# Optimization experiments

Hardware: AMD Instinct MI355X
Metric: run time of the kernel (lower is better)

## Reference

```python
import jax, jax.numpy as jnp
import numpy as np

H = 16  # num_heads
LN_EPS = 1e-5


def setup_inputs() -> dict:
    key = jax.random.key(0)
    ks = jax.random.split(key, 9)
    B, T, D = 2, 2048, 1024
    s = D ** -0.5
    return {
        "q": jax.random.normal(ks[0], (B, T, D), jnp.float32),
        "k": jax.random.normal(ks[1], (B, T, D), jnp.float32),
        "v": jax.random.normal(ks[2], (B, T, D), jnp.float32),
        "wq": jax.random.normal(ks[3], (D, D), jnp.float32) * s,
        "bq": jnp.zeros((D,), jnp.float32),
        "wk": jax.random.normal(ks[4], (D, D), jnp.float32) * s,
        "bk": jnp.zeros((D,), jnp.float32),
        "wv": jax.random.normal(ks[5], (D, D), jnp.float32) * s,
        "bv": jnp.zeros((D,), jnp.float32),
        "ln_g": jnp.ones((D,), jnp.float32),
        "ln_b": jnp.zeros((D,), jnp.float32),
    }


def _layernorm(x, g, b):
    mu = jnp.mean(x, axis=-1, keepdims=True)
    var = jnp.mean(jnp.square(x - mu), axis=-1, keepdims=True)
    return (x - mu) * jax.lax.rsqrt(var + LN_EPS) * g + b


def reference(q, k, v, wq, bq, wk, bk, wv, bv, ln_g, ln_b):
    B, T, D = q.shape
    dh = D // H
    residual = q
    qp = q @ wq.T + bq
    kp = k @ wk.T + bk
    vp = v @ wv.T + bv
    # faithful to torch: flat row-major view (B,T,D) -> (H*B, T, dh)
    qh = qp.reshape(H * B, T, dh)
    kh = kp.reshape(H * B, T, dh)
    vh = vp.reshape(H * B, T, dh)
    scores = jnp.einsum('btd,bsd->bts', qh, kh) * (dh ** -0.5)  # (H*B, T, T)
    attn = jax.nn.softmax(scores, axis=-1)
    ctx = jnp.einsum('bts,bsd->btd', attn, vh)  # (H*B, T, dh)
    ctx = ctx.reshape(B, T, D)
    out = _layernorm(residual + ctx, ln_g, ln_b)
    return (out, attn)
```

## Files before the change

### kernel.cpp

```cpp
#include <hip/hip_runtime.h>

typedef unsigned short u16;
typedef __attribute__((ext_vector_type(8))) short s8v;
typedef __attribute__((ext_vector_type(4))) float f4v;

#define MFMA16(a, b, c) __builtin_amdgcn_mfma_f32_16x16x32_bf16(a, b, c, 0, 0, 0)

#define TSEQ 2048
#define NTOK 4096
#define HEADS 32
#define HB_ELEMS 131072

__device__ __forceinline__ unsigned cvt_pk(float lo, float hi) {
  unsigned r;
  asm("v_cvt_pk_bf16_f32 %0, %1, %2" : "=v"(r) : "v"(lo), "v"(hi));
  return r;
}

__device__ __forceinline__ void gl_lds16(const u16* g, u16* l) {
  __builtin_amdgcn_global_load_lds(
      (const __attribute__((address_space(1))) void*)g,
      (__attribute__((address_space(3))) void*)l, 16, 0, 0);
}

__global__ void cvt_all(const float* __restrict__ q, const float* __restrict__ k,
                        const float* __restrict__ v, const float* __restrict__ wq,
                        const float* __restrict__ wk, const float* __restrict__ wv,
                        u16* __restrict__ dst) {
  int i = (blockIdx.x * blockDim.x + threadIdx.x) * 4;
  const float* src; int off;
  if (i < 12582912) {
    int s = i >> 22; src = (s == 0) ? q : ((s == 1) ? k : v); off = i & 4194303;
  } else {
    int j = i - 12582912;
    int s = j >> 20; src = (s == 0) ? wq : ((s == 1) ? wk : wv); off = j & 1048575;
  }
  float4 val = *(const float4*)(src + off);
  uint2 o;
  o.x = cvt_pk(val.x, val.y);
  o.y = cvt_pk(val.z, val.w);
  *(uint2*)(dst + i) = o;
}

__launch_bounds__(256, 3)
__global__ void proj_gemm(const u16* __restrict__ Aall, const u16* __restrict__ Wall,
                          const float* __restrict__ bqp, const float* __restrict__ bkp,
                          const float* __restrict__ bvp, u16* __restrict__ Call) {
  const int z = blockIdx.z;
  const u16* A = Aall + (size_t)z * 4194304;
  const u16* W = Wall + (size_t)z * 1048576;
  u16* C = Call + (size_t)z * 4194304;
  const float* bias = (z == 0) ? bqp : ((z == 1) ? bkp : bvp);

  __shared__ __align__(16) u16 SH[17408];
  u16* As = SH;
  u16* Bs = SH + 8192;

  const int tid = threadIdx.x;
  const int w = tid >> 6, lane = tid & 63, g = lane >> 4, l = lane & 15;
  const int wr = w >> 1, wc = w & 1;
  const int tr = blockIdx.y * 128, tc = blockIdx.x * 128;

  const int srow = tid >> 3;
  const int scol = (tid & 7) * 8;

  f4v acc[4][4] = {};

  for (int kt = 0; kt < 1024; kt += 64) {
#pragma unroll
    for (int c4 = 0; c4 < 4; ++c4) {
      gl_lds16(A + (size_t)(tr + c4 * 32 + srow) * 1024 + kt + scol,
               As + c4 * 2048 + tid * 8);
      gl_lds16(W + (size_t)(tc + c4 * 32 + srow) * 1024 + kt + scol,
               Bs + c4 * 2048 + tid * 8);
    }
    __syncthreads();
#pragma unroll
    for (int ks = 0; ks < 2; ++ks) {
      s8v a[4], bb[4];
#pragma unroll
      for (int m = 0; m < 4; ++m)
        a[m] = *(const s8v*)(As + (wr * 64 + m * 16 + l) * 64 + ks * 32 + g * 8);
#pragma unroll
      for (int n = 0; n < 4; ++n)
        bb[n] = *(const s8v*)(Bs + (wc * 64 + n * 16 + l) * 64 + ks * 32 + g * 8);
#pragma unroll
      for (int m = 0; m < 4; ++m)
#pragma unroll
        for (int n = 0; n < 4; ++n)
          acc[m][n] = MFMA16(a[m], bb[n], acc[m][n]);
    }
    __syncthreads();
  }
  u16* T = SH;
#pragma unroll
  for (int m = 0; m < 4; ++m)
#pragma unroll
    for (int n = 0; n < 4; ++n) {
      int d = wc * 64 + n * 16 + l;
      float bv = bias[tc + d];
      unsigned c01 = cvt_pk(acc[m][n][0] + bv, acc[m][n][1] + bv);
      unsigned c23 = cvt_pk(acc[m][n][2] + bv, acc[m][n][3] + bv);
      int t0 = wr * 64 + m * 16 + g * 4;
      T[(t0 + 0) * 136 + d] = (u16)c01;
      T[(t0 + 1) * 136 + d] = (u16)(c01 >> 16);
      T[(t0 + 2) * 136 + d] = (u16)c23;
      T[(t0 + 3) * 136 + d] = (u16)(c23 >> 16);
    }
  __syncthreads();
#pragma unroll
  for (int it = 0; it < 8; ++it) {
    int t = it * 16 + (tid >> 4);
    int c8 = (tid & 15) * 8;
    *(s8v*)(C + (size_t)(tr + t) * 1024 + tc + c8) = *(const s8v*)&T[t * 136 + c8];
  }
}

__global__ void vtrans(const u16* __restrict__ vp, u16* __restrict__ vT) {
  const int hb = blockIdx.y;
  const int t0 = blockIdx.x * 64;
  const int tid = threadIdx.x;
  __shared__ u16 tl[64][65];
  const u16* vph = vp + (size_t)hb * HB_ELEMS;
  u16* vth = vT + (size_t)hb * HB_ELEMS;
#pragma unroll
  for (int it = 0; it < 4; ++it) {
    int i = (tid + it * 256) * 4;
    int r = i >> 6, c = i & 63;
    *(ushort4*)&tl[r][c] = *(const ushort4*)(vph + (size_t)(t0 + r) * 64 + c);
  }
  __syncthreads();
#pragma unroll
  for (int it = 0; it < 4; ++it) {
    int i = (tid + it * 256) * 4;
    int d = i >> 6, j = i & 63;
    ushort4 o;
    o.x = tl[j + 0][d]; o.y = tl[j + 1][d]; o.z = tl[j + 2][d]; o.w = tl[j + 3][d];
    *(ushort4*)(vth + (size_t)d * TSEQ + t0 + j) = o;
  }
}

__launch_bounds__(512, 2)
__global__ void attn_fused(const u16* __restrict__ qp, const u16* __restrict__ kp,
                           const u16* __restrict__ vT, float* __restrict__ attn,
                           float* __restrict__ ctx) {
  const int hw = blockIdx.x + (blockIdx.y << 4);
  const int hb = (hw & 7) + ((hw >> 7) << 3);
  const int qt = (hw >> 3) & 15;

  const int tid = threadIdx.x;
  const int w = tid >> 6, lane = tid & 63, g = lane >> 4, l = lane & 15;
  const int lx = l & 7;

  const u16* qh = qp + (size_t)hb * HB_ELEMS;
  const u16* kh = kp + (size_t)hb * HB_ELEMS;
  const u16* vh = vT + (size_t)hb * HB_ELEMS;

  __shared__ __align__(16) u16 SH[27648];

  const int row0 = qt * 128 + w * 16;
  const float scale = 0.125f;

  const int srow = tid >> 3;
  const int swc = ((tid & 7) ^ (srow & 7)) * 8;

  s8v qf0 = *(const s8v*)(qh + (size_t)(row0 + l) * 64 + g * 8);
  s8v qf1 = *(const s8v*)(qh + (size_t)(row0 + l) * 64 + 32 + g * 8);

  float sum = 0.0f;
  for (int kt4 = 0; kt4 < 8; ++kt4) {
    const int c0 = kt4 * 256;
#pragma unroll
    for (int c4 = 0; c4 < 4; ++c4)
      gl_lds16(kh + (size_t)(c0 + c4 * 64 + srow) * 64 + swc,
               SH + c4 * 4096 + tid * 8);
    __syncthreads();
#pragma unroll
    for (int q4 = 0; q4 < 4; ++q4) {
#pragma unroll
      for (int n = 0; n < 4; ++n) {
        const u16* kr = SH + q4 * 4096 + (n * 16 + l) * 64;
        s8v b0 = *(const s8v*)(kr + (g ^ lx) * 8);
        s8v b1 = *(const s8v*)(kr + ((4 + g) ^ lx) * 8);
        f4v s = {};
        s = MFMA16(b0, qf0, s);
        s = MFMA16(b1, qf1, s);
        sum += __expf(s[0] * scale) + __expf(s[1] * scale)
             + __expf(s[2] * scale) + __expf(s[3] * scale);
      }
    }
    __syncthreads();
  }
  sum += __shfl_xor(sum, 16);
  sum += __shfl_xor(sum, 32);
  const float inv = 1.0f / sum;

  u16* Kl = SH;
  u16* Vl = SH + 4096;
  float* Pf = (float*)(SH + 8192);

  f4v cacc[4] = {};
  float* attn_h = attn + (size_t)hb * TSEQ * TSEQ;
  const int kt0 = (qt * 2 + ((hw >> 7) << 3)) & 31;
  const int prow = w * 16 + l;
  const int st_r = tid >> 4;
  const int st_c = (tid & 15) * 4;
  for (int i = 0; i < 32; ++i) {
    const int kt = (i + kt0) & 31;
    const int col0 = kt * 64;
    gl_lds16(kh + (size_t)(col0 + srow) * 64 + swc, Kl + tid * 8);
    gl_lds16(vh + (size_t)srow * TSEQ + col0 + swc, Vl + tid * 8);
    __syncthreads();
#pragma unroll
    for (int n = 0; n < 4; ++n) {
      const u16* kr = Kl + (n * 16 + l) * 64;
      s8v b0 = *(const s8v*)(kr + (g ^ lx) * 8);
      s8v b1 = *(const s8v*)(kr + ((4 + g) ^ lx) * 8);
      f4v s = {};
      s = MFMA16(b0, qf0, s);
      s = MFMA16(b1, qf1, s);
      f4v p;
#pragma unroll
      for (int r = 0; r < 4; ++r) p[r] = __expf(s[r] * scale) * inv;
      *(f4v*)&Pf[prow * 76 + n * 16 + g * 4] = p;
    }
    asm volatile("s_waitcnt lgkmcnt(0)" ::: "memory");
    __builtin_amdgcn_sched_barrier(0);
#pragma unroll
    for (int ks = 0; ks < 2; ++ks) {
      const float* pr = &Pf[prow * 76 + ks * 32 + g * 8];
      f4v r0 = *(const f4v*)pr;
      f4v r1 = *(const f4v*)(pr + 4);
      union { unsigned u[4]; s8v s; } pc;
      pc.u[0] = cvt_pk(r0[0], r0[1]);
      pc.u[1] = cvt_pk(r0[2], r0[3]);
      pc.u[2] = cvt_pk(r1[0], r1[1]);
      pc.u[3] = cvt_pk(r1[2], r1[3]);
      s8v pa = pc.s;
#pragma unroll
      for (int n4 = 0; n4 < 4; ++n4) {
        const u16* vr = Vl + (n4 * 16 + l) * 64;
        s8v bvv = *(const s8v*)(vr + ((ks * 4 + g) ^ lx) * 8);
        cacc[n4] = MFMA16(pa, bvv, cacc[n4]);
      }
    }
    __syncthreads();
#pragma unroll
    for (int r4 = 0; r4 < 4; ++r4) {
      const int rho = r4 * 32 + st_r;
      f4v pv_ = *(const f4v*)&Pf[rho * 76 + st_c];
      *(f4v*)(attn_h + (size_t)(qt * 128 + rho) * TSEQ + col0 + st_c) = pv_;
    }
  }
#pragma unroll
  for (int n4 = 0; n4 < 4; ++n4)
#pragma unroll
    for (int r = 0; r < 4; ++r)
      ctx[(size_t)hb * HB_ELEMS + (size_t)(row0 + g * 4 + r) * 64 + n4 * 16 + l] =
          cacc[n4][r];
}

__global__ void ln_kernel(const float* __restrict__ q, const float* __restrict__ ctx,
                          const float* __restrict__ gam, const float* __restrict__ bet,
                          float* __restrict__ out) {
  const int row = blockIdx.x;
  const int tid = threadIdx.x;
  const float* qr = q + (size_t)row * 1024;
  const float* cr = ctx + (size_t)row * 1024;
  float4 xq = *(const float4*)(qr + tid * 4);
  float4 xc = *(const float4*)(cr + tid * 4);
  float x0 = xq.x + xc.x, x1 = xq.y + xc.y, x2 = xq.z + xc.z, x3 = xq.w + xc.w;
  float s1 = x0 + x1 + x2 + x3;
  float s2 = x0 * x0 + x1 * x1 + x2 * x2 + x3 * x3;
#pragma unroll
  for (int off = 1; off < 64; off <<= 1) {
    s1 += __shfl_xor(s1, off);
    s2 += __shfl_xor(s2, off);
  }
  __shared__ float ra[4], rb[4];
  int w = tid >> 6, lane = tid & 63;
  if (lane == 0) { ra[w] = s1; rb[w] = s2; }
  __syncthreads();
  s1 = ra[0] + ra[1] + ra[2] + ra[3];
  s2 = rb[0] + rb[1] + rb[2] + rb[3];
  float mu = s1 * (1.0f / 1024.0f);
  float var = s2 * (1.0f / 1024.0f) - mu * mu;
  float rstd = rsqrtf(var + 1e-5f);
  float4 gv = *(const float4*)(gam + tid * 4);
  float4 bv = *(const float4*)(bet + tid * 4);
  float4 o;
  o.x = (x0 - mu) * rstd * gv.x + bv.x;
  o.y = (x1 - mu) * rstd * gv.y + bv.y;
  o.z = (x2 - mu) * rstd * gv.z + bv.z;
  o.w = (x3 - mu) * rstd * gv.w + bv.w;
  *(float4*)(out + (size_t)row * 1024 + tid * 4) = o;
}

extern "C" void kernel_launch(void* const* d_in, const int* in_sizes, int n_in,
                              void* d_out, int out_size, void* d_ws, size_t ws_size,
                              hipStream_t stream) {
  const float* q    = (const float*)d_in[0];
  const float* k    = (const float*)d_in[1];
  const float* v    = (const float*)d_in[2];
  const float* wq   = (const float*)d_in[3];
  const float* bq   = (const float*)d_in[4];
  const float* wk   = (const float*)d_in[5];
  const float* bk   = (const float*)d_in[6];
  const float* wv   = (const float*)d_in[7];
  const float* bv   = (const float*)d_in[8];
  const float* ln_g = (const float*)d_in[9];
  const float* ln_b = (const float*)d_in[10];

  char* ws = (char*)d_ws;
  u16* qbf  = (u16*)(ws);
  u16* wbf  = (u16*)(ws + 25165824);
  u16* qp   = (u16*)(ws + 31457280);
  u16* vT   = (u16*)(ws + 56623104);
  float* ctx = (float*)(ws + 65011712);

  float* out  = (float*)d_out;
  float* attn = out + 4194304;

  cvt_all<<<15360, 256, 0, stream>>>(q, k, v, wq, wk, wv, qbf);

  proj_gemm<<<dim3(8, 32, 3), 256, 0, stream>>>(qbf, wbf, bq, bk, bv, qp);

  vtrans<<<dim3(32, 32), 256, 0, stream>>>(qp + 8388608, vT);

  attn_fused<<<dim3(16, 32), 512, 0, stream>>>(qp, qp + 4194304, vT, attn, ctx);

  ln_kernel<<<4096, 256, 0, stream>>>(q, ctx, ln_g, ln_b, out);
}
```

Before: 222.4 us.

## Double-buffer K/V tiles and make attn stores warp-local to drop a barrier

Allocates two LDS buffers for K and V tiles in the second pass and prefetches the next tile while the current one is computed, replacing two __syncthreads per iteration with a single barrier. That barrier waits on vmcnt(4) so the four outstanding attn stores do not block it. The attn store from LDS is remapped so each warp writes only its own 16 P rows, which removes the barrier between the PV MFMA and the store. LDS usage grows from about 54KB to about 70KB per block, which may affect the 2-blocks-per-CU occupancy target.

```diff
diff --git a/kernel.cpp b/kernel.cpp
--- a/kernel.cpp
+++ b/kernel.cpp
@@ -156,7 +156,7 @@
   const u16* kh = kp + (size_t)hb * HB_ELEMS;
   const u16* vh = vT + (size_t)hb * HB_ELEMS;
 
-  __shared__ __align__(16) u16 SH[27648];
+  __shared__ __align__(16) u16 SH[35840];
 
   const int row0 = qt * 128 + w * 16;
   const float scale = 0.125f;
@@ -194,23 +194,35 @@
   sum += __shfl_xor(sum, 16);
   sum += __shfl_xor(sum, 32);
   const float inv = 1.0f / sum;
-
-  u16* Kl = SH;
-  u16* Vl = SH + 4096;
-  float* Pf = (float*)(SH + 8192);
+  __syncthreads();
+
+  u16* K0 = SH;
+  u16* V0 = SH + 8192;
+  float* Pf = (float*)(SH + 16384);
+
+#define STAGE2(b, kt_) do { const int c0_ = (kt_) * 64;                          \
+    gl_lds16(kh + (size_t)(c0_ + srow) * 64 + swc, K0 + (b) * 4096 + tid * 8);   \
+    gl_lds16(vh + (size_t)srow * TSEQ + c0_ + swc, V0 + (b) * 4096 + tid * 8);   \
+  } while (0)
 
   f4v cacc[4] = {};
   float* attn_h = attn + (size_t)hb * TSEQ * TSEQ;
   const int kt0 = (qt * 2 + ((hw >> 7) << 3)) & 31;
   const int prow = w * 16 + l;
-  const int st_r = tid >> 4;
-  const int st_c = (tid & 15) * 4;
+  const int sr4 = lane >> 4;
+  const int sc = (lane & 15) * 4;
+
+  STAGE2(0, kt0);
+  asm volatile("s_waitcnt vmcnt(0)" ::: "memory");
+  __builtin_amdgcn_sched_barrier(0);
+  __builtin_amdgcn_s_barrier();
+
   for (int i = 0; i < 32; ++i) {
-    const int kt = (i + kt0) & 31;
-    const int col0 = kt * 64;
-    gl_lds16(kh + (size_t)(col0 + srow) * 64 + swc, Kl + tid * 8);
-    gl_lds16(vh + (size_t)srow * TSEQ + col0 + swc, Vl + tid * 8);
-    __syncthreads();
+    const int cur = i & 1;
+    const int col0 = ((i + kt0) & 31) * 64;
+    const u16* Kl = K0 + cur * 4096;
+    const u16* Vl = V0 + cur * 4096;
+    if (i < 31) STAGE2(cur ^ 1, (i + 1 + kt0) & 31);
 #pragma unroll
     for (int n = 0; n < 4; ++n) {
       const u16* kr = Kl + (n * 16 + l) * 64;
@@ -244,14 +256,20 @@
         cacc[n4] = MFMA16(pa, bvv, cacc[n4]);
       }
     }
-    __syncthreads();
 #pragma unroll
     for (int r4 = 0; r4 < 4; ++r4) {
-      const int rho = r4 * 32 + st_r;
-      f4v pv_ = *(const f4v*)&Pf[rho * 76 + st_c];
-      *(f4v*)(attn_h + (size_t)(qt * 128 + rho) * TSEQ + col0 + st_c) = pv_;
-    }
-  }
+      const int row = w * 16 + r4 * 4 + sr4;
+      f4v pv_ = *(const f4v*)&Pf[row * 76 + sc];
+      *(f4v*)(attn_h + (size_t)(qt * 128 + row) * TSEQ + col0 + sc) = pv_;
+    }
+    if (i < 31) {
+      asm volatile("s_waitcnt lgkmcnt(0)" ::: "memory");
+      asm volatile("s_waitcnt vmcnt(4)" ::: "memory");
+      __builtin_amdgcn_sched_barrier(0);
+      __builtin_amdgcn_s_barrier();
+    }
+  }
+#undef STAGE2
 #pragma unroll
   for (int n4 = 0; n4 < 4; ++n4)
 #pragma unroll
```

New measurement: 213.5 us. 4.0% less time.
